# Performance work log

Measured on AMD Instinct MI355X. Metric: run time of the kernel, lower is better.

## Reference

```python
import jax, jax.numpy as jnp
import numpy as np

B, L, D_MODEL, HEADS = 4, 2048, 1024, 16
D_K = D_MODEL // HEADS
EPS = 1e-8
ROPE_BASE = 10000.0


def setup_inputs() -> dict:
    key = jax.random.key(0)
    k1, k2, k3 = jax.random.split(key, 3)
    x = jax.random.normal(k1, (B, L, D_MODEL), jnp.float32)
    W_in = jax.random.normal(k2, (3 * D_MODEL, D_MODEL), jnp.float32) * 0.02
    W_o = jax.random.normal(k3, (D_MODEL, D_MODEL), jnp.float32) * 0.02
    return {"x": x, "W_in": W_in, "W_o": W_o}


def _layer_norm(x, eps=EPS):
    # F.layer_norm with no affine params
    mu = jnp.mean(x, axis=-1, keepdims=True)
    var = jnp.var(x, axis=-1, keepdims=True)
    return (x - mu) * jax.lax.rsqrt(var + eps)


def _rope(x):
    # x: [B, H, L, d_k]; interleaved-pair rotary embedding
    seq = x.shape[2]
    half = x.shape[-1] // 2
    inv_freq = 1.0 / (ROPE_BASE ** (jnp.arange(half, dtype=jnp.float32) * 2.0 / x.shape[-1]))
    ang = jnp.arange(seq, dtype=jnp.float32)[:, None] * inv_freq[None, :]  # [L, half]
    cos, sin = jnp.cos(ang), jnp.sin(ang)
    x1, x2 = x[..., 0::2], x[..., 1::2]
    r1 = x1 * cos - x2 * sin
    r2 = x1 * sin + x2 * cos
    return jnp.stack([r1, r2], axis=-1).reshape(x.shape)


def reference(x, W_in, W_o):
    h = _layer_norm(x)
    qkv = h @ W_in.T  # [B, L, 3*D]
    q, k, v = jnp.split(qkv, 3, axis=-1)
    to_heads = lambda t: t.reshape(B, L, HEADS, D_K).transpose(0, 2, 1, 3)  # [B,H,L,dk]
    q, k, v = to_heads(q), to_heads(k), to_heads(v)
    q, k = _rope(q), _rope(k)
    scale = 1.0 / np.sqrt(D_K).astype(np.float32)
    scores = jnp.einsum('bhqd,bhkd->bhqk', q, k) * scale
    causal = jnp.tril(jnp.ones((L, L), dtype=bool))
    scores = jnp.where(causal, scores, -jnp.inf)
    attn = jax.nn.softmax(scores, axis=-1)
    o = jnp.einsum('bhqk,bhkd->bhqd', attn, v)
    o = o.transpose(0, 2, 1, 3).reshape(B, L, D_MODEL)
    return o @ W_o.T
```

## Files before the change

### kernel.cpp

```cpp
#include <hip/hip_runtime.h>
#include <cstdint>

typedef unsigned short u16;
typedef short bf16x8 __attribute__((ext_vector_type(8)));
typedef float f32x4 __attribute__((ext_vector_type(4)));
typedef float f32x16 __attribute__((ext_vector_type(16)));
typedef unsigned int u32x2 __attribute__((ext_vector_type(2)));
typedef unsigned int u32x4 __attribute__((ext_vector_type(4)));

#define NB 4
#define SEQ 2048
#define DMODEL 1024
#define NHEADS 16
#define DHEAD 64
#define BHTOT (NB*NHEADS)
#define MROWS (NB*SEQ)

__device__ __forceinline__ float bf2f(u16 u){
  union { unsigned int i; float f; } x; x.i = ((unsigned int)u)<<16; return x.f;
}
__device__ __forceinline__ u16 f2bf(float f){
  union { float f; unsigned int i; } x; x.f = f;
  unsigned int r = x.i + 0x7fffu + ((x.i>>16)&1u);
  return (u16)(r>>16);
}

typedef const __attribute__((address_space(1))) unsigned int* gas_t;
typedef __attribute__((address_space(3))) unsigned int* las_t;
__device__ __forceinline__ void async_cp16(const void* g, void* l){
  __builtin_amdgcn_global_load_lds((gas_t)g, (las_t)l, 16, 0, 0);
}

__device__ __forceinline__ void plswap(unsigned int &a, unsigned int &b){
#if __has_builtin(__builtin_amdgcn_permlane32_swap)
  u32x2 r = __builtin_amdgcn_permlane32_swap(a, b, false, false);
  a = r[0]; b = r[1];
#else
  asm("v_permlane32_swap_b32 %0, %1" : "+v"(a), "+v"(b));
#endif
}

__global__ __launch_bounds__(256) void cast2_kernel(const float* __restrict__ wa, u16* __restrict__ oa,
    const float* __restrict__ wb, u16* __restrict__ ob, int na4){
  int i = blockIdx.x*256 + threadIdx.x;
  const float* src; u16* dst; int j;
  if(i < na4){ src = wa; dst = oa; j = i; }
  else       { src = wb; dst = ob; j = i - na4; }
  float4 v = ((const float4*)src)[j];
  ushort4 o;
  o.x=f2bf(v.x); o.y=f2bf(v.y); o.z=f2bf(v.z); o.w=f2bf(v.w);
  ((ushort4*)dst)[j] = o;
}

__global__ __launch_bounds__(256) void ln_kernel(const float* __restrict__ x, u16* __restrict__ h){
  int row = blockIdx.x;
  const float* xr = x + (size_t)row*DMODEL;
  u16* hr = h + (size_t)row*DMODEL;
  int t = threadIdx.x;
  float4 v = ((const float4*)xr)[t];
  float f0=v.x, f1=v.y, f2=v.z, f3=v.w;
  float s = f0+f1+f2+f3;
  float q = f0*f0+f1*f1+f2*f2+f3*f3;
  #pragma unroll
  for(int off=32; off; off>>=1){ s += __shfl_xor(s, off); q += __shfl_xor(q, off); }
  __shared__ float ss[4], sq[4];
  int wv = t>>6, lane = t&63;
  if(lane==0){ ss[wv]=s; sq[wv]=q; }
  __syncthreads();
  s = ss[0]+ss[1]+ss[2]+ss[3];
  q = sq[0]+sq[1]+sq[2]+sq[3];
  float mu  = s * (1.0f/DMODEL);
  float var = q * (1.0f/DMODEL) - mu*mu;
  float rs  = rsqrtf(var + 1e-8f);
  ushort4 o;
  o.x=f2bf((f0-mu)*rs); o.y=f2bf((f1-mu)*rs); o.z=f2bf((f2-mu)*rs); o.w=f2bf((f3-mu)*rs);
  ((ushort4*)hr)[t] = o;
}

#define BM 128
#define BN 128
#define BK 32

template<int MODE>
__global__ __launch_bounds__(256) void gemm_bt(const u16* __restrict__ A, const u16* __restrict__ Bm,
    u16* __restrict__ Qb, u16* __restrict__ Kb, u16* __restrict__ Vtb, float* __restrict__ outf,
    int M, int N, int K){
  __shared__ u16 As[2][BM*BK];
  __shared__ u16 Bs[2][BN*BK];
  int t = threadIdx.x;
  int lane = t&63, wv = t>>6;
  int c = lane&15, g = lane>>4;
  int wm = wv>>1, wn = wv&1;
  int m0 = blockIdx.y*BM, n0 = blockIdx.x*BN;

  int p0 = t>>3,        j0 = t&7;        int js0 = j0 ^ (p0&7);
  int p1 = (t+256)>>3,  j1 = t&7;        int js1 = j1 ^ (p1&7);
  size_t aoff0 = (size_t)(p0*2 + (js0>>2))*K + (js0&3)*8;
  size_t aoff1 = (size_t)(p1*2 + (js1>>2))*K + (js1&3)*8;
  const u16* Abase = A  + (size_t)m0*K;
  const u16* Bbase = Bm + (size_t)n0*K;

  f32x4 acc[4][4] = {};

  async_cp16(Abase + aoff0, &As[0][t*8]);
  async_cp16(Abase + aoff1, &As[0][(t+256)*8]);
  async_cp16(Bbase + aoff0, &Bs[0][t*8]);
  async_cp16(Bbase + aoff1, &Bs[0][(t+256)*8]);

  int cur = 0;
  for(int k0=0;k0<K;k0+=BK){
    __syncthreads();
    if(k0+BK < K){
      int nb = cur^1;
      async_cp16(Abase + (k0+BK) + aoff0, &As[nb][t*8]);
      async_cp16(Abase + (k0+BK) + aoff1, &As[nb][(t+256)*8]);
      async_cp16(Bbase + (k0+BK) + aoff0, &Bs[nb][t*8]);
      async_cp16(Bbase + (k0+BK) + aoff1, &Bs[nb][(t+256)*8]);
    }
    bf16x8 af[4], bfr[4];
    #pragma unroll
    for(int i=0;i<4;i++){
      int ra = wm*64 + i*16 + c;
      int qa = ((ra&1)*4 + g) ^ ((ra>>1)&7);
      af[i]  = *(const bf16x8*)(&As[cur][(ra>>1)*64 + qa*8]);
      int rb = wn*64 + i*16 + c;
      int qb = ((rb&1)*4 + g) ^ ((rb>>1)&7);
      bfr[i] = *(const bf16x8*)(&Bs[cur][(rb>>1)*64 + qb*8]);
    }
    #pragma unroll
    for(int mi=0;mi<4;mi++)
      #pragma unroll
      for(int ni=0;ni<4;ni++)
        acc[mi][ni] = __builtin_amdgcn_mfma_f32_16x16x32_bf16(af[mi], bfr[ni], acc[mi][ni], 0,0,0);
    cur ^= 1;
  }
  if(MODE==1){
    #pragma unroll
    for(int mi=0;mi<4;mi++){
      int mrow = m0 + wm*64 + mi*16 + g*4;
      #pragma unroll
      for(int ni=0;ni<4;ni++){
        int ncol = n0 + wn*64 + ni*16 + c;
        #pragma unroll
        for(int r=0;r<4;r++)
          outf[(size_t)(mrow+r)*N + ncol] = acc[mi][ni][r];
      }
    }
  } else {
    #pragma unroll
    for(int ni=0;ni<4;ni++){
      int n = n0 + wn*64 + ni*16 + c;
      int sel = n>>10, head = (n>>6)&15, d = n&63;
      #pragma unroll
      for(int mi=0;mi<4;mi++){
        int m = m0 + wm*64 + mi*16 + g*4;
        int b = m>>11, l = m&(SEQ-1);
        if(sel<2){
          u16* dst = (sel==0?Qb:Kb) + ((size_t)((b*NHEADS+head)*SEQ + l))*DHEAD + d;
          #pragma unroll
          for(int r=0;r<4;r++) dst[(size_t)r*DHEAD] = f2bf(acc[mi][ni][r]);
        } else {
          ushort4 pk;
          pk.x=f2bf(acc[mi][ni][0]); pk.y=f2bf(acc[mi][ni][1]);
          pk.z=f2bf(acc[mi][ni][2]); pk.w=f2bf(acc[mi][ni][3]);
          *(ushort4*)(&Vtb[((size_t)((b*NHEADS+head)*DHEAD + d))*SEQ + l]) = pk;
        }
      }
    }
  }
}

#define SC2 0.180336879f
__global__ __launch_bounds__(256) void rope_kernel(u16* __restrict__ Q, u16* __restrict__ Kb){
  int tid = blockIdx.x*256 + threadIdx.x;
  int j = tid&31, l = tid>>5;
  float inv = exp2f(-(float)j * (13.28771237954945f/32.0f));
  float sn, cs;
  sincosf((float)l*inv, &sn, &cs);
  size_t base = (size_t)l*DHEAD + 2*j;
  #pragma unroll 4
  for(int bh=0; bh<BHTOT; bh++){
    size_t off = base + (size_t)bh*SEQ*DHEAD;
    ushort2 q2 = *(ushort2*)(&Q[off]);
    float x1=bf2f(q2.x), x2=bf2f(q2.y);
    ushort2 o;
    o.x = f2bf((x1*cs - x2*sn)*SC2); o.y = f2bf((x1*sn + x2*cs)*SC2);
    *(ushort2*)(&Q[off]) = o;
    ushort2 k2 = *(ushort2*)(&Kb[off]);
    x1=bf2f(k2.x); x2=bf2f(k2.y);
    o.x = f2bf(x1*cs - x2*sn); o.y = f2bf(x1*sn + x2*cs);
    *(ushort2*)(&Kb[off]) = o;
  }
}


#define QKS32(KF) { \
  f32x16 z_ = {}; \
  z_ = __builtin_amdgcn_mfma_f32_32x32x16_bf16(KF[0], qf[0], z_, 0,0,0); \
  z_ = __builtin_amdgcn_mfma_f32_32x32x16_bf16(KF[1], qf[1], z_, 0,0,0); \
  z_ = __builtin_amdgcn_mfma_f32_32x32x16_bf16(KF[2], qf[2], z_, 0,0,0); \
  z_ = __builtin_amdgcn_mfma_f32_32x32x16_bf16(KF[3], qf[3], z_, 0,0,0); \
  sc = z_; }

#define LDK { \
  _Pragma("unroll") for(int dk_=0;dk_<4;dk_++){ \
    int kb_ = (c32*128 + dk_*32 + hl*16) ^ ((c32&7)<<4); \
    kf[dk_] = *(const bf16x8*)((const char*)(&Kls[cur][0]) + kb_); } }

#define LDV { \
  _Pragma("unroll") for(int dt_=0;dt_<2;dt_++) \
    _Pragma("unroll") for(int ks_=0;ks_<2;ks_++){ \
      int d_ = dt_*32 + c32; \
      int vb_ = (d_*64 + ks_*32 + hl*16) ^ (((d_>>1)&7)<<4); \
      vf[dt_][ks_] = *(const bf16x8*)((const char*)(&Vls[cur][0]) + vb_); } }

#define EXPPACK(MASKED) { \
  unsigned int pk_[8]; \
  _Pragma("unroll") for(int j_=0;j_<8;j_++){ \
    float a_ = exp2f(sc[2*j_]); \
    float b_ = exp2f(sc[2*j_+1]); \
    if(MASKED){ \
      int k0_ = ((2*j_)&3)   + 8*((2*j_)>>2)   + 4*hl; \
      int k1_ = ((2*j_+1)&3) + 8*((2*j_+1)>>2) + 4*hl; \
      a_ = (k0_ <= c32) ? a_ : 0.f; \
      b_ = (k1_ <= c32) ? b_ : 0.f; } \
    lrow += a_ + b_; \
    asm("v_cvt_pk_bf16_f32 %0, %1, %2" : "=v"(pk_[j_]) : "v"(a_), "v"(b_)); } \
  plswap(pk_[0], pk_[2]); \
  plswap(pk_[1], pk_[3]); \
  plswap(pk_[4], pk_[6]); \
  plswap(pk_[5], pk_[7]); \
  u32x4 wa_ = { pk_[0], pk_[1], pk_[2], pk_[3] }; \
  u32x4 wb_ = { pk_[4], pk_[5], pk_[6], pk_[7] }; \
  pa0 = __builtin_bit_cast(bf16x8, wa_); \
  pa1 = __builtin_bit_cast(bf16x8, wb_); }

#define PVM32 { \
  oacc0 = __builtin_amdgcn_mfma_f32_32x32x16_bf16(pa0, vf[0][0], oacc0, 0,0,0); \
  oacc0 = __builtin_amdgcn_mfma_f32_32x32x16_bf16(pa1, vf[0][1], oacc0, 0,0,0); \
  oacc1 = __builtin_amdgcn_mfma_f32_32x32x16_bf16(pa0, vf[1][0], oacc1, 0,0,0); \
  oacc1 = __builtin_amdgcn_mfma_f32_32x32x16_bf16(pa1, vf[1][1], oacc1, 0,0,0); }

__global__ __launch_bounds__(512, 4) void attn_kernel(const u16* __restrict__ Q, const u16* __restrict__ Kb,
    const u16* __restrict__ Vt, u16* __restrict__ O){
  __shared__ u16 Kls[2][2048];
  __shared__ u16 Vls[2][2048];
  __shared__ float Ls[8][32];
  int t = threadIdx.x, lane = t&63, w = t>>6;
  int c32 = lane&31, hl = lane>>5, h8 = hl*8;
  int bh = blockIdx.x;
  int b = bh>>4, hh = bh&15;
  int g = 7 - blockIdx.y;
  int s = g*8 + w;
  int wrow = s*32;
  int NT = g*8 + 8;
  const u16* Qp = Q  + (size_t)bh*SEQ*DHEAD;
  const u16* Kp = Kb + (size_t)bh*SEQ*DHEAD;
  const u16* Vp = Vt + (size_t)bh*DHEAD*SEQ;

  bool isK = (w < 4);
  int cch = isK ? t : (t - 256);
  int prow = cch>>3;
  int jsrc = (cch&7) ^ (prow&7);
  size_t soff0, sstep;
  if(isK){
    soff0 = (size_t)prow*64 + (size_t)jsrc*8;
    sstep = 32*64;
  } else {
    int c2 = prow*8 + jsrc;
    soff0 = (size_t)(c2>>2)*SEQ + (size_t)(c2&3)*8;
    sstep = 32;
  }
  const u16* sbase = isK ? Kp : Vp;

  bf16x8 qf[4];
  #pragma unroll
  for(int dk=0;dk<4;dk++)
    qf[dk] = *(const bf16x8*)(&Qp[(size_t)(wrow + c32)*DHEAD + dk*16 + h8]);

  f32x16 oacc0 = {}, oacc1 = {};
  float lrow = 0.f;
  f32x16 sc;
  bf16x8 kf[4], vf[2][2], pa0, pa1;

  {
    u16* dst = isK ? &Kls[0][cch*8] : &Vls[0][cch*8];
    async_cp16(sbase + soff0, dst);
  }
  int cur = 0;
  #pragma unroll 1
  for(int tt=0; tt<NT; ++tt){
    __syncthreads();
    if(tt+1 < NT){
      u16* dst = isK ? &Kls[cur^1][cch*8] : &Vls[cur^1][cch*8];
      async_cp16(sbase + soff0 + (size_t)(tt+1)*sstep, dst);
    }
    if(tt <= s){
      LDK; LDV;
      QKS32(kf);
      if(tt == s){ EXPPACK(1); } else { EXPPACK(0); }
      PVM32;
    }
    cur ^= 1;
  }

  float lr = lrow + __shfl_xor(lrow, 32);
  __syncthreads();
  if(hl==0) Ls[w][c32] = lr;
  __syncthreads();
  #pragma unroll
  for(int r=0;r<16;r++){
    int row = (r&3)+8*(r>>2)+4*hl;
    float linv = 1.0f/Ls[w][row];
    size_t o = ((size_t)(b*SEQ + wrow + row))*DMODEL + hh*DHEAD;
    O[o + c32]      = f2bf(oacc0[r]*linv);
    O[o + 32 + c32] = f2bf(oacc1[r]*linv);
  }
}

extern "C" void kernel_launch(void* const* d_in, const int* in_sizes, int n_in,
                              void* d_out, int out_size, void* d_ws, size_t ws_size,
                              hipStream_t stream){
  const float* x    = (const float*)d_in[0];
  const float* W_in = (const float*)d_in[1];
  const float* W_o  = (const float*)d_in[2];
  u16* ws = (u16*)d_ws;
  const size_t T16 = (size_t)8*1024*1024;
  u16* h   = ws;
  u16* Qb  = ws +   T16;
  u16* Kb  = ws + 2*T16;
  u16* Vtb = ws + 3*T16;
  u16* Wb  = ws + 4*T16;
  u16* Wob = Wb + (size_t)3*DMODEL*DMODEL;
  u16* Ob  = h;
  float* out = (float*)d_out;

  const int na4 = 3*DMODEL*DMODEL/4;
  const int nb4 = DMODEL*DMODEL/4;
  cast2_kernel<<<dim3((na4+nb4)/256), dim3(256), 0, stream>>>(W_in, Wb, W_o, Wob, na4);
  ln_kernel<<<dim3(MROWS), dim3(256), 0, stream>>>(x, h);
  gemm_bt<0><<<dim3(3*DMODEL/BN, MROWS/BM), dim3(256), 0, stream>>>(
      h, Wb, Qb, Kb, Vtb, nullptr, MROWS, 3*DMODEL, DMODEL);
  rope_kernel<<<dim3(SEQ*32/256), dim3(256), 0, stream>>>(Qb, Kb);
  attn_kernel<<<dim3(BHTOT, 8), dim3(512), 0, stream>>>(Qb, Kb, Vtb, Ob);
  gemm_bt<1><<<dim3(DMODEL/BN, MROWS/BM), dim3(256), 0, stream>>>(
      Ob, Wob, nullptr, nullptr, nullptr, out, MROWS, DMODEL, DMODEL);
}
```

Baseline: 274.3 us.

## Pair mirrored causal query tiles per warp to balance work and reuse K/V

Each warp now handles two query tiles, one near the start and its mirror near the end of the sequence, so every block does the same amount of causal work. Each K/V tile staged in shared memory feeds both tiles' score and PV MFMAs. The grid is halved along y and launch bounds drop to 2 blocks per CU. This adds register pressure from the doubled accumulators and Q fragments, and halves the number of blocks in flight.

```diff
diff --git a/kernel.cpp b/kernel.cpp
--- a/kernel.cpp
+++ b/kernel.cpp
@@ -194,12 +194,12 @@
 }
 
 
-#define QKS32(KF) { \
+#define QKS32(QF) { \
   f32x16 z_ = {}; \
-  z_ = __builtin_amdgcn_mfma_f32_32x32x16_bf16(KF[0], qf[0], z_, 0,0,0); \
-  z_ = __builtin_amdgcn_mfma_f32_32x32x16_bf16(KF[1], qf[1], z_, 0,0,0); \
-  z_ = __builtin_amdgcn_mfma_f32_32x32x16_bf16(KF[2], qf[2], z_, 0,0,0); \
-  z_ = __builtin_amdgcn_mfma_f32_32x32x16_bf16(KF[3], qf[3], z_, 0,0,0); \
+  z_ = __builtin_amdgcn_mfma_f32_32x32x16_bf16(kf[0], QF[0], z_, 0,0,0); \
+  z_ = __builtin_amdgcn_mfma_f32_32x32x16_bf16(kf[1], QF[1], z_, 0,0,0); \
+  z_ = __builtin_amdgcn_mfma_f32_32x32x16_bf16(kf[2], QF[2], z_, 0,0,0); \
+  z_ = __builtin_amdgcn_mfma_f32_32x32x16_bf16(kf[3], QF[3], z_, 0,0,0); \
   sc = z_; }
 
 #define LDK { \
@@ -214,7 +214,7 @@
       int vb_ = (d_*64 + ks_*32 + hl*16) ^ (((d_>>1)&7)<<4); \
       vf[dt_][ks_] = *(const bf16x8*)((const char*)(&Vls[cur][0]) + vb_); } }
 
-#define EXPPACK(MASKED) { \
+#define EXPPACK(MASKED, LROW) { \
   unsigned int pk_[8]; \
   _Pragma("unroll") for(int j_=0;j_<8;j_++){ \
     float a_ = exp2f(sc[2*j_]); \
@@ -224,7 +224,7 @@
       int k1_ = ((2*j_+1)&3) + 8*((2*j_+1)>>2) + 4*hl; \
       a_ = (k0_ <= c32) ? a_ : 0.f; \
       b_ = (k1_ <= c32) ? b_ : 0.f; } \
-    lrow += a_ + b_; \
+    LROW += a_ + b_; \
     asm("v_cvt_pk_bf16_f32 %0, %1, %2" : "=v"(pk_[j_]) : "v"(a_), "v"(b_)); } \
   plswap(pk_[0], pk_[2]); \
   plswap(pk_[1], pk_[3]); \
@@ -235,25 +235,26 @@
   pa0 = __builtin_bit_cast(bf16x8, wa_); \
   pa1 = __builtin_bit_cast(bf16x8, wb_); }
 
-#define PVM32 { \
-  oacc0 = __builtin_amdgcn_mfma_f32_32x32x16_bf16(pa0, vf[0][0], oacc0, 0,0,0); \
-  oacc0 = __builtin_amdgcn_mfma_f32_32x32x16_bf16(pa1, vf[0][1], oacc0, 0,0,0); \
-  oacc1 = __builtin_amdgcn_mfma_f32_32x32x16_bf16(pa0, vf[1][0], oacc1, 0,0,0); \
-  oacc1 = __builtin_amdgcn_mfma_f32_32x32x16_bf16(pa1, vf[1][1], oacc1, 0,0,0); }
-
-__global__ __launch_bounds__(512, 4) void attn_kernel(const u16* __restrict__ Q, const u16* __restrict__ Kb,
+#define PVM32(O0, O1) { \
+  O0 = __builtin_amdgcn_mfma_f32_32x32x16_bf16(pa0, vf[0][0], O0, 0,0,0); \
+  O0 = __builtin_amdgcn_mfma_f32_32x32x16_bf16(pa1, vf[0][1], O0, 0,0,0); \
+  O1 = __builtin_amdgcn_mfma_f32_32x32x16_bf16(pa0, vf[1][0], O1, 0,0,0); \
+  O1 = __builtin_amdgcn_mfma_f32_32x32x16_bf16(pa1, vf[1][1], O1, 0,0,0); }
+
+__global__ __launch_bounds__(512, 2) void attn_kernel(const u16* __restrict__ Q, const u16* __restrict__ Kb,
     const u16* __restrict__ Vt, u16* __restrict__ O){
   __shared__ u16 Kls[2][2048];
   __shared__ u16 Vls[2][2048];
-  __shared__ float Ls[8][32];
+  __shared__ float LsA[8][32];
+  __shared__ float LsB[8][32];
   int t = threadIdx.x, lane = t&63, w = t>>6;
   int c32 = lane&31, hl = lane>>5, h8 = hl*8;
   int bh = blockIdx.x;
   int b = bh>>4, hh = bh&15;
-  int g = 7 - blockIdx.y;
-  int s = g*8 + w;
-  int wrow = s*32;
-  int NT = g*8 + 8;
+  int y = blockIdx.y;
+  int sA = 8*y + w;
+  int sB = 63 - 8*y - w;
+  int NT = 64 - 8*y;
   const u16* Qp = Q  + (size_t)bh*SEQ*DHEAD;
   const u16* Kp = Kb + (size_t)bh*SEQ*DHEAD;
   const u16* Vp = Vt + (size_t)bh*DHEAD*SEQ;
@@ -273,13 +274,15 @@
   }
   const u16* sbase = isK ? Kp : Vp;
 
-  bf16x8 qf[4];
+  bf16x8 qfA[4], qfB[4];
   #pragma unroll
-  for(int dk=0;dk<4;dk++)
-    qf[dk] = *(const bf16x8*)(&Qp[(size_t)(wrow + c32)*DHEAD + dk*16 + h8]);
-
-  f32x16 oacc0 = {}, oacc1 = {};
-  float lrow = 0.f;
+  for(int dk=0;dk<4;dk++){
+    qfA[dk] = *(const bf16x8*)(&Qp[(size_t)(sA*32 + c32)*DHEAD + dk*16 + h8]);
+    qfB[dk] = *(const bf16x8*)(&Qp[(size_t)(sB*32 + c32)*DHEAD + dk*16 + h8]);
+  }
+
+  f32x16 oaccA0 = {}, oaccA1 = {}, oaccB0 = {}, oaccB1 = {};
+  float lrowA = 0.f, lrowB = 0.f;
   f32x16 sc;
   bf16x8 kf[4], vf[2][2], pa0, pa1;
 
@@ -295,26 +298,36 @@
       u16* dst = isK ? &Kls[cur^1][cch*8] : &Vls[cur^1][cch*8];
       async_cp16(sbase + soff0 + (size_t)(tt+1)*sstep, dst);
     }
-    if(tt <= s){
+    if(tt <= sB){
       LDK; LDV;
-      QKS32(kf);
-      if(tt == s){ EXPPACK(1); } else { EXPPACK(0); }
-      PVM32;
+      QKS32(qfB);
+      if(tt == sB){ EXPPACK(1, lrowB); } else { EXPPACK(0, lrowB); }
+      PVM32(oaccB0, oaccB1);
+      if(tt <= sA){
+        QKS32(qfA);
+        if(tt == sA){ EXPPACK(1, lrowA); } else { EXPPACK(0, lrowA); }
+        PVM32(oaccA0, oaccA1);
+      }
     }
     cur ^= 1;
   }
 
-  float lr = lrow + __shfl_xor(lrow, 32);
+  float lrA = lrowA + __shfl_xor(lrowA, 32);
+  float lrB = lrowB + __shfl_xor(lrowB, 32);
   __syncthreads();
-  if(hl==0) Ls[w][c32] = lr;
+  if(hl==0){ LsA[w][c32] = lrA; LsB[w][c32] = lrB; }
   __syncthreads();
   #pragma unroll
   for(int r=0;r<16;r++){
     int row = (r&3)+8*(r>>2)+4*hl;
-    float linv = 1.0f/Ls[w][row];
-    size_t o = ((size_t)(b*SEQ + wrow + row))*DMODEL + hh*DHEAD;
-    O[o + c32]      = f2bf(oacc0[r]*linv);
-    O[o + 32 + c32] = f2bf(oacc1[r]*linv);
+    float livA = 1.0f/LsA[w][row];
+    float livB = 1.0f/LsB[w][row];
+    size_t oA = ((size_t)(b*SEQ + sA*32 + row))*DMODEL + hh*DHEAD;
+    size_t oB = ((size_t)(b*SEQ + sB*32 + row))*DMODEL + hh*DHEAD;
+    O[oA + c32]      = f2bf(oaccA0[r]*livA);
+    O[oA + 32 + c32] = f2bf(oaccA1[r]*livA);
+    O[oB + c32]      = f2bf(oaccB0[r]*livB);
+    O[oB + 32 + c32] = f2bf(oaccB1[r]*livB);
   }
 }
 
@@ -342,7 +355,7 @@
   gemm_bt<0><<<dim3(3*DMODEL/BN, MROWS/BM), dim3(256), 0, stream>>>(
       h, Wb, Qb, Kb, Vtb, nullptr, MROWS, 3*DMODEL, DMODEL);
   rope_kernel<<<dim3(SEQ*32/256), dim3(256), 0, stream>>>(Qb, Kb);
-  attn_kernel<<<dim3(BHTOT, 8), dim3(512), 0, stream>>>(Qb, Kb, Vtb, Ob);
+  attn_kernel<<<dim3(BHTOT, 4), dim3(512), 0, stream>>>(Qb, Kb, Vtb, Ob);
   gemm_bt<1><<<dim3(DMODEL/BN, MROWS/BM), dim3(256), 0, stream>>>(
       Ob, Wob, nullptr, nullptr, nullptr, out, MROWS, DMODEL, DMODEL);
 }
```

Result: no change. 272.5 us (-0.6%).
